# Kernel optimization log

Measured on AMD Instinct MI355X. Metric: run time of the kernel, lower is better.

Reference implementation:

```python
import jax, jax.numpy as jnp
import numpy as np

M = 2_097_152
C = 32
R = 256

# Same plane_axes buffer as the torch module (3 permutation matrices).
PLANE_AXES = jnp.array(
    [[[0, 1, 0], [1, 0, 0], [0, 0, 1]],
     [[0, 0, 1], [1, 0, 0], [0, 1, 0]],
     [[0, 1, 0], [0, 0, 1], [1, 0, 0]]], dtype=jnp.float32)


def setup_inputs() -> dict:
    key = jax.random.key(0)
    k1, k2 = jax.random.split(key)
    xyz = jax.random.uniform(k1, (M, 3), dtype=jnp.float32, minval=-1.0, maxval=1.0)
    # rand_init: triplane = randn * 0.001
    triplane = jax.random.normal(k2, (3, C, R, R), dtype=jnp.float32) * 0.001
    return {"xyz": xyz, "triplane": triplane}


def _grid_sample_bilinear(plane, coords):
    """plane: (C,H,W); coords: (M,2) normalized (x,y) in [-1,1].
    Matches torch F.grid_sample(mode='bilinear', padding_mode='zeros',
    align_corners=True). Returns (M,C)."""
    Cc, H, W = plane.shape
    ix = (coords[:, 0] + 1.0) * 0.5 * (W - 1)  # x indexes width
    iy = (coords[:, 1] + 1.0) * 0.5 * (H - 1)  # y indexes height
    x0 = jnp.floor(ix)
    y0 = jnp.floor(iy)
    x1 = x0 + 1.0
    y1 = y0 + 1.0
    wx1 = ix - x0
    wx0 = 1.0 - wx1
    wy1 = iy - y0
    wy0 = 1.0 - wy1

    def tap(xf, yf, w):
        valid = (xf >= 0) & (xf <= W - 1) & (yf >= 0) & (yf <= H - 1)
        xi = jnp.clip(xf, 0, W - 1).astype(jnp.int32)
        yi = jnp.clip(yf, 0, H - 1).astype(jnp.int32)
        v = plane[:, yi, xi]  # (C, M) gather
        return v * (w * valid.astype(w.dtype))[None, :]

    out = (tap(x0, y0, wx0 * wy0) + tap(x1, y0, wx1 * wy0)
           + tap(x0, y1, wx0 * wy1) + tap(x1, y1, wx1 * wy1))  # (C, M)
    return out.T  # (M, C)


def reference(xyz, triplane):
    # project_onto_planes: xyz @ inv(plane_axes), keep first two coords
    inv_planes = jnp.linalg.inv(PLANE_AXES)             # (3,3,3)
    proj = jnp.einsum('md,pdk->pmk', xyz, inv_planes)[..., :2]  # (3,M,2)
    feats = jax.vmap(_grid_sample_bilinear)(triplane, proj)      # (3,M,C)
    return feats.sum(axis=0)  # (M,C)
```

## Files before the change

### kernel.cpp

```cpp
#include <hip/hip_runtime.h>

#define R 256
#define C 32
#define NBIN 64
#define CAPB 40960
#define PPB 1024

typedef float f32x4 __attribute__((ext_vector_type(4)));

__device__ __forceinline__ int bin_of(float px, float py, float pz) {
    int cx = min(max((int)((px + 1.0f) * 2.0f), 0), 3);
    int cy = min(max((int)((py + 1.0f) * 2.0f), 0), 3);
    int cz = min(max((int)((pz + 1.0f) * 2.0f), 0), 3);
    int oct = ((cz >> 1) << 2) | ((cy >> 1) << 1) | (cx >> 1);
    int sub = ((cz & 1) << 2) | ((cy & 1) << 1) | (cx & 1);
    return (oct << 3) | sub;
}

__device__ __forceinline__ void convert_body(const float* __restrict__ tri,
                                             ushort* __restrict__ tw, int bid) {
    int p = bid >> 8;
    int y = bid & (R - 1);
    int x = threadIdx.x;

    unsigned packed[C / 2];
#pragma unroll
    for (int i = 0; i < C / 2; ++i) {
        unsigned w = 0;
#pragma unroll
        for (int h = 0; h < 2; ++h) {
            float f = tri[(((p * C + (2 * i + h)) * R) + y) * R + x];
            unsigned u = __float_as_uint(f);
            unsigned r = (u + 0x7fffu + ((u >> 16) & 1u)) >> 16;
            w |= (r & 0xffffu) << (16 * h);
        }
        packed[i] = w;
    }
    uint4* dst = (uint4*)(tw + ((size_t)(p * R + y) * R + x) * C);
#pragma unroll
    for (int i = 0; i < 4; ++i) {
        dst[i] = make_uint4(packed[4 * i], packed[4 * i + 1],
                            packed[4 * i + 2], packed[4 * i + 3]);
    }
}

__global__ __launch_bounds__(256) void convert_scatter_kernel(
        const float* __restrict__ tri, ushort* __restrict__ tw,
        const float* __restrict__ xyz, unsigned* __restrict__ acnt,
        unsigned* __restrict__ ovcnt, f32x4* __restrict__ arena,
        f32x4* __restrict__ ov, int M) {
    int bid = blockIdx.x;
    if (bid < 3 * R) {
        convert_body(tri, tw, bid);
        return;
    }

    __shared__ unsigned lcnt[NBIN], lbase[NBIN], gbase[NBIN], lofs[NBIN];
    __shared__ f32x4 stag[PPB];
    __shared__ unsigned char sbin[PPB];

    int t = threadIdx.x;
    if (t < NBIN) { lcnt[t] = 0u; lofs[t] = 0u; }
    __syncthreads();

    int base = (bid - 3 * R) * PPB;
    float pxl[4], pyl[4], pzl[4];
    int   bl[4];
#pragma unroll
    for (int k = 0; k < 4; ++k) {
        int m = base + k * 256 + t;
        bl[k] = -1;
        if (m < M) {
            pxl[k] = xyz[3 * m + 0];
            pyl[k] = xyz[3 * m + 1];
            pzl[k] = xyz[3 * m + 2];
            bl[k]  = bin_of(pxl[k], pyl[k], pzl[k]);
            atomicAdd(&lcnt[bl[k]], 1u);
        }
    }
    __syncthreads();

    if (t < NBIN) {
        unsigned x   = lcnt[t];
        unsigned inc = x;
#pragma unroll
        for (int d = 1; d < NBIN; d <<= 1) {
            unsigned v = __shfl_up(inc, d);
            if (t >= d) inc += v;
        }
        lbase[t] = inc - x;
        gbase[t] = atomicAdd(&acnt[t], x);
    }
    __syncthreads();

#pragma unroll
    for (int k = 0; k < 4; ++k) {
        if (bl[k] >= 0) {
            unsigned slot = atomicAdd(&lofs[bl[k]], 1u);
            unsigned j    = lbase[bl[k]] + slot;
            int m = base + k * 256 + t;
            f32x4 rec = {pxl[k], pyl[k], pzl[k], __int_as_float(m)};
            stag[j] = rec;
            sbin[j] = (unsigned char)bl[k];
        }
    }
    __syncthreads();

    int tot = (int)(lbase[NBIN - 1] + lcnt[NBIN - 1]);
    for (int j = t; j < tot; j += 256) {
        int b = sbin[j];
        unsigned pos = gbase[b] + ((unsigned)j - lbase[b]);
        f32x4 rec = stag[j];
        if (pos < CAPB) arena[(size_t)b * CAPB + pos] = rec;
        else            ov[atomicAdd(ovcnt, 1u)] = rec;
    }
}

__global__ __launch_bounds__(256) void convert_kernel(const float* __restrict__ tri,
                                                      ushort* __restrict__ tw) {
    convert_body(tri, tw, blockIdx.x);
}

__device__ __forceinline__ void tap_fma(uint4 v, float w, float* acc) {
    unsigned d[4] = {v.x, v.y, v.z, v.w};
#pragma unroll
    for (int k = 0; k < 4; ++k) {
        acc[2 * k]     = fmaf(w, __uint_as_float(d[k] << 16),          acc[2 * k]);
        acc[2 * k + 1] = fmaf(w, __uint_as_float(d[k] & 0xffff0000u), acc[2 * k + 1]);
    }
}

__device__ __forceinline__ void sample_point(float px, float py, float pz, int mo,
                                             const ushort* __restrict__ twc,
                                             float* __restrict__ out, int cq) {
    float uu[3] = {py, pz, py};
    float vv[3] = {px, px, pz};

    float acc[8];
#pragma unroll
    for (int j = 0; j < 8; ++j) acc[j] = 0.0f;

#pragma unroll
    for (int p = 0; p < 3; ++p) {
        float ix = (uu[p] + 1.0f) * 0.5f * 255.0f;
        float iy = (vv[p] + 1.0f) * 0.5f * 255.0f;
        int   x0 = (int)ix;
        int   y0 = (int)iy;
        float wx1 = ix - (float)x0;
        float wy1 = iy - (float)y0;
        float wx0 = 1.0f - wx1;
        float wy0 = 1.0f - wy1;
        int x1 = min(x0 + 1, R - 1);
        int y1 = min(y0 + 1, R - 1);

        float w00 = wx0 * wy0, w01 = wx1 * wy0, w10 = wx0 * wy1, w11 = wx1 * wy1;

        const ushort* pl = twc + (size_t)p * R * R * C;
        uint4 v00 = *(const uint4*)(pl + (y0 * R + x0) * C);
        uint4 v01 = *(const uint4*)(pl + (y0 * R + x1) * C);
        uint4 v10 = *(const uint4*)(pl + (y1 * R + x0) * C);
        uint4 v11 = *(const uint4*)(pl + (y1 * R + x1) * C);

        tap_fma(v00, w00, acc);
        tap_fma(v01, w01, acc);
        tap_fma(v10, w10, acc);
        tap_fma(v11, w11, acc);
    }

    f32x4* o = (f32x4*)(out + (size_t)mo * C + 8 * cq);
    f32x4 o0 = {acc[0], acc[1], acc[2], acc[3]};
    f32x4 o1 = {acc[4], acc[5], acc[6], acc[7]};
    __builtin_nontemporal_store(o0, o);
    __builtin_nontemporal_store(o1, o + 1);
}

__global__ __launch_bounds__(256) void sample_bins(const f32x4* __restrict__ arena,
                                                   const unsigned* __restrict__ acnt,
                                                   const unsigned* __restrict__ ovcnt,
                                                   const f32x4* __restrict__ ov,
                                                   const ushort* __restrict__ tw,
                                                   float* __restrict__ out) {
    int bid = blockIdx.x;
    int oct = bid & 7;
    int sub = (bid >> 3) & 7;
    int w   = bid >> 6;
    int bin = oct * 8 + sub;

    int quad = threadIdx.x >> 2;
    int cq   = threadIdx.x & 3;
    const ushort* twc = tw + 8 * cq;

    int n = min((int)acnt[bin], CAPB);
    const f32x4* bk = arena + (size_t)bin * CAPB;
    for (int i = w * 64 + quad; i < n; i += 32 * 64) {
        f32x4 r = __builtin_nontemporal_load(bk + i);
        sample_point(r.x, r.y, r.z, __float_as_int(r.w), twc, out, cq);
    }

    int nov = (int)*ovcnt;
    if (nov > 0) {
        int gq = (bid * 256 + (int)threadIdx.x) >> 2;
        for (int j = gq; j < nov; j += 2048 * 64) {
            f32x4 r = ov[j];
            sample_point(r.x, r.y, r.z, __float_as_int(r.w), twc, out, cq);
        }
    }
}

__global__ __launch_bounds__(256) void sample_kernel(const float* __restrict__ xyz,
                                                     const ushort* __restrict__ tw,
                                                     float* __restrict__ out, int M) {
    int tid = blockIdx.x * 256 + threadIdx.x;
    int q   = tid >> 2;
    int cq  = tid & 3;
    int nq  = (gridDim.x * 256) >> 2;
    const ushort* twc = tw + 8 * cq;
    for (int m = q; m < M; m += nq) {
        float px = xyz[3 * m + 0], py = xyz[3 * m + 1], pz = xyz[3 * m + 2];
        sample_point(px, py, pz, m, twc, out, cq);
    }
}

extern "C" void kernel_launch(void* const* d_in, const int* in_sizes, int n_in,
                              void* d_out, int out_size, void* d_ws, size_t ws_size,
                              hipStream_t stream) {
    const float* xyz = (const float*)d_in[0];
    const float* tri = (const float*)d_in[1];
    float* out = (float*)d_out;

    int M = in_sizes[0] / 3;

    size_t tw_bytes = (size_t)3 * R * R * C * sizeof(ushort);
    size_t cnt_off  = tw_bytes;
    size_t arena_off = cnt_off + 256;
    size_t ov_off   = arena_off + (size_t)NBIN * CAPB * sizeof(f32x4);
    size_t need     = ov_off + (size_t)M * sizeof(f32x4);

    ushort*   tw    = (ushort*)d_ws;
    unsigned* acnt  = (unsigned*)((char*)d_ws + cnt_off);
    unsigned* ovcnt = acnt + NBIN;
    f32x4*    arena = (f32x4*)((char*)d_ws + arena_off);
    f32x4*    ov    = (f32x4*)((char*)d_ws + ov_off);

    if (ws_size >= need) {
        hipMemsetAsync(acnt, 0, 256, stream);
        int sb = (M + PPB - 1) / PPB;
        convert_scatter_kernel<<<3 * R + sb, 256, 0, stream>>>(
            tri, tw, xyz, acnt, ovcnt, arena, ov, M);
        sample_bins<<<2048, 256, 0, stream>>>(arena, acnt, ovcnt, ov, tw, out);
    } else {
        convert_kernel<<<3 * R, 256, 0, stream>>>(tri, tw);
        sample_kernel<<<4096, 256, 0, stream>>>(xyz, tw, out, M);
    }
}
```

Baseline: 447.0 us.

## Pad bin counters, issue all gathers before FMAs, prefetch next arena record

Each bin's global counter now sits on its own 64-byte line, so atomics from the scatter blocks no longer contend on shared cache lines. The sampler issues all twelve bilinear tap loads before any FMA, exposing more memory-level parallelism. The bin loop software-prefetches the next point record while the current point is being sampled. These raise register pressure, which may lower occupancy, and enlarge the counter region that gets memset.

```diff
diff --git a/kernel.cpp b/kernel.cpp
--- a/kernel.cpp
+++ b/kernel.cpp
@@ -5,6 +5,7 @@
 #define NBIN 64
 #define CAPB 40960
 #define PPB 1024
+#define CNTP 16
 
 typedef float f32x4 __attribute__((ext_vector_type(4)));
 
@@ -89,7 +90,7 @@
             if (t >= d) inc += v;
         }
         lbase[t] = inc - x;
-        gbase[t] = atomicAdd(&acnt[t], x);
+        gbase[t] = atomicAdd(&acnt[t * CNTP], x);
     }
     __syncthreads();
 
@@ -136,10 +137,8 @@
     float uu[3] = {py, pz, py};
     float vv[3] = {px, px, pz};
 
-    float acc[8];
-#pragma unroll
-    for (int j = 0; j < 8; ++j) acc[j] = 0.0f;
-
+    uint4 v[12];
+    float wt[12];
 #pragma unroll
     for (int p = 0; p < 3; ++p) {
         float ix = (uu[p] + 1.0f) * 0.5f * 255.0f;
@@ -153,19 +152,22 @@
         int x1 = min(x0 + 1, R - 1);
         int y1 = min(y0 + 1, R - 1);
 
-        float w00 = wx0 * wy0, w01 = wx1 * wy0, w10 = wx0 * wy1, w11 = wx1 * wy1;
-
         const ushort* pl = twc + (size_t)p * R * R * C;
-        uint4 v00 = *(const uint4*)(pl + (y0 * R + x0) * C);
-        uint4 v01 = *(const uint4*)(pl + (y0 * R + x1) * C);
-        uint4 v10 = *(const uint4*)(pl + (y1 * R + x0) * C);
-        uint4 v11 = *(const uint4*)(pl + (y1 * R + x1) * C);
-
-        tap_fma(v00, w00, acc);
-        tap_fma(v01, w01, acc);
-        tap_fma(v10, w10, acc);
-        tap_fma(v11, w11, acc);
-    }
+        v[4 * p + 0] = *(const uint4*)(pl + (y0 * R + x0) * C);
+        v[4 * p + 1] = *(const uint4*)(pl + (y0 * R + x1) * C);
+        v[4 * p + 2] = *(const uint4*)(pl + (y1 * R + x0) * C);
+        v[4 * p + 3] = *(const uint4*)(pl + (y1 * R + x1) * C);
+        wt[4 * p + 0] = wx0 * wy0;
+        wt[4 * p + 1] = wx1 * wy0;
+        wt[4 * p + 2] = wx0 * wy1;
+        wt[4 * p + 3] = wx1 * wy1;
+    }
+
+    float acc[8];
+#pragma unroll
+    for (int j = 0; j < 8; ++j) acc[j] = 0.0f;
+#pragma unroll
+    for (int s = 0; s < 12; ++s) tap_fma(v[s], wt[s], acc);
 
     f32x4* o = (f32x4*)(out + (size_t)mo * C + 8 * cq);
     f32x4 o0 = {acc[0], acc[1], acc[2], acc[3]};
@@ -190,11 +192,22 @@
     int cq   = threadIdx.x & 3;
     const ushort* twc = tw + 8 * cq;
 
-    int n = min((int)acnt[bin], CAPB);
+    int n = min((int)acnt[bin * CNTP], CAPB);
     const f32x4* bk = arena + (size_t)bin * CAPB;
-    for (int i = w * 64 + quad; i < n; i += 32 * 64) {
+
+    int i = w * 64 + quad;
+    if (i < n) {
         f32x4 r = __builtin_nontemporal_load(bk + i);
-        sample_point(r.x, r.y, r.z, __float_as_int(r.w), twc, out, cq);
+        while (true) {
+            int inext = i + 32 * 64;
+            bool more = inext < n;
+            f32x4 rn;
+            if (more) rn = __builtin_nontemporal_load(bk + inext);
+            sample_point(r.x, r.y, r.z, __float_as_int(r.w), twc, out, cq);
+            if (!more) break;
+            r = rn;
+            i = inext;
+        }
     }
 
     int nov = (int)*ovcnt;
@@ -230,20 +243,21 @@
 
     int M = in_sizes[0] / 3;
 
-    size_t tw_bytes = (size_t)3 * R * R * C * sizeof(ushort);
-    size_t cnt_off  = tw_bytes;
-    size_t arena_off = cnt_off + 256;
-    size_t ov_off   = arena_off + (size_t)NBIN * CAPB * sizeof(f32x4);
-    size_t need     = ov_off + (size_t)M * sizeof(f32x4);
+    size_t tw_bytes  = (size_t)3 * R * R * C * sizeof(ushort);
+    size_t cnt_off   = tw_bytes;
+    size_t cnt_bytes = (size_t)NBIN * CNTP * sizeof(unsigned) + 128;
+    size_t arena_off = cnt_off + ((cnt_bytes + 255) & ~(size_t)255);
+    size_t ov_off    = arena_off + (size_t)NBIN * CAPB * sizeof(f32x4);
+    size_t need      = ov_off + (size_t)M * sizeof(f32x4);
 
     ushort*   tw    = (ushort*)d_ws;
     unsigned* acnt  = (unsigned*)((char*)d_ws + cnt_off);
-    unsigned* ovcnt = acnt + NBIN;
+    unsigned* ovcnt = acnt + NBIN * CNTP;
     f32x4*    arena = (f32x4*)((char*)d_ws + arena_off);
     f32x4*    ov    = (f32x4*)((char*)d_ws + ov_off);
 
     if (ws_size >= need) {
-        hipMemsetAsync(acnt, 0, 256, stream);
+        hipMemsetAsync(acnt, 0, cnt_bytes, stream);
         int sb = (M + PPB - 1) / PPB;
         convert_scatter_kernel<<<3 * R + sb, 256, 0, stream>>>(
             tri, tw, xyz, acnt, ovcnt, arena, ov, M);
```

New measurement: 439.6 us. No clear change (-1.7%).
